# Kernel tuning notes

Measured on AMD Instinct MI355X. Metric: run time of the kernel, lower is better.

Reference implementation:

```python
import jax, jax.numpy as jnp
import numpy as np

N_NODES = 50000
N_EDGES = 800000
D = 128
N_GRAPHS = 64
N_CLASSES = 10


def setup_inputs() -> dict:
    key = jax.random.key(0)
    ks = jax.random.split(key, 10)
    x = jax.random.normal(ks[0], (N_NODES, D), dtype=jnp.float32)
    edge_index = jax.random.randint(ks[1], (2, N_EDGES), 0, N_NODES, dtype=jnp.int64)
    batch = jnp.sort(jax.random.randint(ks[2], (N_NODES,), 0, N_GRAPHS, dtype=jnp.int64))
    s = 1.0 / np.sqrt(D)
    W1a = jax.random.uniform(ks[3], (D, D), jnp.float32, -s, s)
    W1b = jax.random.uniform(ks[4], (D, D), jnp.float32, -s, s)
    W2a = jax.random.uniform(ks[5], (D, D), jnp.float32, -s, s)
    W2b = jax.random.uniform(ks[6], (D, D), jnp.float32, -s, s)
    Wfc = jax.random.uniform(ks[7], (D, N_CLASSES), jnp.float32, -s, s)
    return {
        "x": x, "edge_index": edge_index, "batch": batch,
        "W1a": W1a, "b1a": jnp.zeros((D,), jnp.float32),
        "W1b": W1b, "b1b": jnp.zeros((D,), jnp.float32),
        "W2a": W2a, "b2a": jnp.zeros((D,), jnp.float32),
        "W2b": W2b, "b2b": jnp.zeros((D,), jnp.float32),
        "Wfc": Wfc, "bfc": jnp.zeros((N_CLASSES,), jnp.float32),
    }


def _gin_conv(x, src, dst, Wa, ba, Wb, bb):
    # sum aggregation of neighbor messages x[src] into dst (eps = 0)
    agg = jax.ops.segment_sum(x[src], dst, num_segments=N_NODES)
    h = x + agg  # (1 + eps) * x + sum_{j->i} x_j
    h = jax.nn.relu(h @ Wa + ba)
    h = jax.nn.relu(h @ Wb + bb)
    return h


def reference(x, edge_index, batch, W1a, b1a, W1b, b1b, W2a, b2a, W2b, b2b, Wfc, bfc):
    src, dst = edge_index[0], edge_index[1]
    h = _gin_conv(x, src, dst, W1a, b1a, W1b, b1b)
    h = _gin_conv(h, src, dst, W2a, b2a, W2b, b2b)
    # global mean pool over graphs
    sums = jax.ops.segment_sum(h, batch, num_segments=N_GRAPHS)
    counts = jax.ops.segment_sum(jnp.ones((h.shape[0], 1), h.dtype), batch, num_segments=N_GRAPHS)
    pooled = sums / jnp.maximum(counts, 1.0)
    logits = pooled @ Wfc + bfc
    return jax.nn.sigmoid(logits)
```

## Files before the change

### kernel.cpp

```cpp
#include <hip/hip_runtime.h>

#define NN 50000
#define NE 800000
#define DF 128
#define NG 64
#define NC 10
#define NBK 98
#define PART_CHUNK 4096
#define PART_GRID 196
#define ACAP 12288
#define FINE_CAP 12288
#define RT 136
#define CAST_GRID 6250
#define PREP_GRID (CAST_GRID + 32)
#define POOL_GRID 391

typedef short bf16x8 __attribute__((ext_vector_type(8)));
typedef float f32x4  __attribute__((ext_vector_type(4)));

__device__ __forceinline__ void atomAddF(float* p, float v) {
  __hip_atomic_fetch_add(p, v, __ATOMIC_RELAXED, __HIP_MEMORY_SCOPE_AGENT);
}
__device__ __forceinline__ float b2f(unsigned short u) {
  union { unsigned int i; float f; } v; v.i = (unsigned int)u << 16; return v.f;
}
__device__ __forceinline__ unsigned int f2b(float f) {
  unsigned int i = __float_as_uint(f);
  return (i + 0x7fffu + ((i >> 16) & 1u)) >> 16;
}

__global__ __launch_bounds__(256) void k_prep_part(const float* __restrict__ x,
                                                   unsigned short* __restrict__ xb,
                                                   const float* __restrict__ W0,
                                                   const float* __restrict__ W1,
                                                   const float* __restrict__ W2,
                                                   const float* __restrict__ W3,
                                                   unsigned short* __restrict__ Wt,
                                                   const int* __restrict__ src,
                                                   const int* __restrict__ dst,
                                                   int* __restrict__ cnt_b,
                                                   unsigned int* __restrict__ arena)
{
  __shared__ unsigned int stage[PART_CHUNK];
  __shared__ int lhist[128], lcnt[128], lcur[128], gbase[128];
  const int tid = threadIdx.x;
  const int b   = blockIdx.x;

  if (b < CAST_GRID) {
    const int i = b * 256 + tid;
    const float4 v = reinterpret_cast<const float4*>(x)[i];
    uint2 o;
    o.x = f2b(v.x) | (f2b(v.y) << 16);
    o.y = f2b(v.z) | (f2b(v.w) << 16);
    reinterpret_cast<uint2*>(xb)[i] = o;
    return;
  }
  if (b < PREP_GRID) {
    const int o = (b - CAST_GRID) * 256 + tid;
    const int mat = o >> 11;
    const float* W = (mat == 0) ? W0 : (mat == 1) ? W1 : (mat == 2) ? W2 : W3;
    const int rem = o & 2047;
    const int kb = rem >> 7, n = rem & 127;
    unsigned int u[8];
#pragma unroll
    for (int j = 0; j < 8; ++j) u[j] = f2b(W[(size_t)(kb * 8 + j) * DF + n]);
    uint4 p;
    p.x = u[0] | (u[1] << 16);
    p.y = u[2] | (u[3] << 16);
    p.z = u[4] | (u[5] << 16);
    p.w = u[6] | (u[7] << 16);
    *reinterpret_cast<uint4*>(Wt + (size_t)mat * DF * DF + (size_t)rem * 8) = p;
    return;
  }

  const int vb = b - PREP_GRID;
  const int e0 = vb * PART_CHUNK;
  const int nE = min(PART_CHUNK, NE - e0);

  for (int i = tid; i < 128; i += 256) lhist[i] = 0;
  __syncthreads();
  unsigned int pk[16]; int bk[16];
#pragma unroll
  for (int i = 0; i < 16; ++i) {
    const int e = e0 + i * 256 + tid;
    if (e < NE) {
      const int d = dst[e], s = src[e];
      const int bb = d >> 9;
      bk[i] = bb;
      pk[i] = ((unsigned int)bb << 25) | ((unsigned int)(d & 511) << 16) | (unsigned int)s;
      atomicAdd(&lhist[bb], 1);
    } else bk[i] = -1;
  }
  __syncthreads();
  for (int i = tid; i < 128; i += 256) lcnt[i] = lhist[i];
  __syncthreads();
  for (int off = 1; off < 128; off <<= 1) {
    int v = 0;
    if (tid < 128 && tid >= off) v = lhist[tid - off];
    __syncthreads();
    if (tid < 128) lhist[tid] += v;
    __syncthreads();
  }
  if (tid < 128) lcur[tid] = lhist[tid] - lcnt[tid];
  __syncthreads();
#pragma unroll
  for (int i = 0; i < 16; ++i)
    if (bk[i] >= 0) {
      const int pos = atomicAdd(&lcur[bk[i]], 1);
      stage[pos] = pk[i];
    }
  __syncthreads();
  if (tid < NBK) {
    const int c = lcnt[tid];
    if (c > 0) gbase[tid] = atomicAdd(&cnt_b[tid], c);
  }
  __syncthreads();
  for (int idx = tid; idx < nE; idx += 256) {
    const unsigned int p = stage[idx];
    const int bb = (int)(p >> 25);
    const int loff = lhist[bb] - lcnt[bb];
    arena[(size_t)bb * ACAP + gbase[bb] + (idx - loff)] = p;
  }
}

__global__ __launch_bounds__(256) void k_fine(const unsigned int* __restrict__ arena,
                                              const int* __restrict__ cnt_b,
                                              int* __restrict__ rs,
                                              unsigned short* __restrict__ es)
{
  __shared__ unsigned short les[FINE_CAP];
  __shared__ int bins[4096];
  __shared__ int partials[256];
  __shared__ int basebuf[128];
  const int tid = threadIdx.x;
  const int b   = blockIdx.x;

  if (b == 0 && tid == 0) rs[NN] = NE;

  if (tid < 128) basebuf[tid] = (tid < NBK) ? cnt_b[tid] : 0;
  __syncthreads();
  for (int off = 1; off < 128; off <<= 1) {
    int u = 0;
    if (tid < 128 && tid >= off) u = basebuf[tid - off];
    __syncthreads();
    if (tid < 128) basebuf[tid] += u;
    __syncthreads();
  }
  const int wbase = (b == 0) ? 0 : basebuf[b - 1];
  const int cnt   = cnt_b[b];
  const int nbase = b << 9;
  const int nwin  = min(512, NN - nbase);
  const unsigned int* ap = arena + (size_t)b * ACAP;

  for (int i = tid; i < 4096; i += 256) bins[i] = 0;
  __syncthreads();
  for (int idx = tid; idx < cnt; idx += 256) {
    const unsigned int p = ap[idx];
    const int key = (int)(((p >> 16) & 511) << 3) | (int)((p & 0xffffu) >> 13);
    atomicAdd(&bins[key], 1);
  }
  __syncthreads();
  const int b16 = tid * 16;
  int sum = 0;
#pragma unroll
  for (int k = 0; k < 16; ++k) sum += bins[b16 + k];
  partials[tid] = sum;
  __syncthreads();
  for (int off = 1; off < 256; off <<= 1) {
    int u = (tid >= off) ? partials[tid - off] : 0;
    __syncthreads();
    partials[tid] += u;
    __syncthreads();
  }
  int run = partials[tid] - sum;
#pragma unroll
  for (int k = 0; k < 16; ++k) {
    const int v = bins[b16 + k];
    bins[b16 + k] = run;
    run += v;
  }
  __syncthreads();
  for (int i = tid; i < nwin; i += 256) rs[nbase + i] = wbase + bins[i << 3];
  __syncthreads();
  if (cnt <= FINE_CAP) {
    for (int idx = tid; idx < cnt; idx += 256) {
      const unsigned int p = ap[idx];
      const int key = (int)(((p >> 16) & 511) << 3) | (int)((p & 0xffffu) >> 13);
      const int pos = atomicAdd(&bins[key], 1);
      les[pos] = (unsigned short)(p & 0xffffu);
    }
    __syncthreads();
    for (int i = tid; i < cnt; i += 256) es[wbase + i] = les[i];
  } else {
    for (int idx = tid; idx < cnt; idx += 256) {
      const unsigned int p = ap[idx];
      const int key = (int)(((p >> 16) & 511) << 3) | (int)((p & 0xffffu) >> 13);
      const int pos = atomicAdd(&bins[key], 1);
      es[wbase + pos] = (unsigned short)(p & 0xffffu);
    }
  }
}

__global__ __launch_bounds__(256) void k_gather(const unsigned short* __restrict__ feat,
                                                unsigned short* __restrict__ outp,
                                                const int* __restrict__ rs,
                                                const unsigned short* __restrict__ es)
{
  const int wid  = (blockIdx.x * 256 + threadIdx.x) >> 6;
  const int lane = threadIdx.x & 63;
  if (wid >= NN) return;
  const int half = lane >> 5;
  const int l32  = lane & 31;
  const int off  = l32 * 4;
  const int beg = rs[wid];
  const int end = rs[wid + 1];

  float a0 = 0.f, a1 = 0.f, a2 = 0.f, a3 = 0.f;
  if (!half) {
    const uint2 u = *reinterpret_cast<const uint2*>(feat + (size_t)wid * DF + off);
    a0 = b2f(u.x & 0xffff); a1 = b2f(u.x >> 16);
    a2 = b2f(u.y & 0xffff); a3 = b2f(u.y >> 16);
  }

  int j = beg;
  for (; j + 7 < end; j += 8) {
    const int i0 = es[j + half];
    const int i1 = es[j + 2 + half];
    const int i2 = es[j + 4 + half];
    const int i3 = es[j + 6 + half];
    const uint2 u0 = *reinterpret_cast<const uint2*>(feat + (size_t)i0 * DF + off);
    const uint2 u1 = *reinterpret_cast<const uint2*>(feat + (size_t)i1 * DF + off);
    const uint2 u2 = *reinterpret_cast<const uint2*>(feat + (size_t)i2 * DF + off);
    const uint2 u3 = *reinterpret_cast<const uint2*>(feat + (size_t)i3 * DF + off);
    a0 += b2f(u0.x & 0xffff) + b2f(u1.x & 0xffff) + b2f(u2.x & 0xffff) + b2f(u3.x & 0xffff);
    a1 += b2f(u0.x >> 16)    + b2f(u1.x >> 16)    + b2f(u2.x >> 16)    + b2f(u3.x >> 16);
    a2 += b2f(u0.y & 0xffff) + b2f(u1.y & 0xffff) + b2f(u2.y & 0xffff) + b2f(u3.y & 0xffff);
    a3 += b2f(u0.y >> 16)    + b2f(u1.y >> 16)    + b2f(u2.y >> 16)    + b2f(u3.y >> 16);
  }
  for (; j + 1 < end; j += 2) {
    const int i = es[j + half];
    const uint2 u = *reinterpret_cast<const uint2*>(feat + (size_t)i * DF + off);
    a0 += b2f(u.x & 0xffff); a1 += b2f(u.x >> 16);
    a2 += b2f(u.y & 0xffff); a3 += b2f(u.y >> 16);
  }
  if (j < end && !half) {
    const int i = es[j];
    const uint2 u = *reinterpret_cast<const uint2*>(feat + (size_t)i * DF + off);
    a0 += b2f(u.x & 0xffff); a1 += b2f(u.x >> 16);
    a2 += b2f(u.y & 0xffff); a3 += b2f(u.y >> 16);
  }

  a0 += __shfl_xor(a0, 32);
  a1 += __shfl_xor(a1, 32);
  a2 += __shfl_xor(a2, 32);
  a3 += __shfl_xor(a3, 32);

  if (!half) {
    uint2 o;
    o.x = f2b(a0) | (f2b(a1) << 16);
    o.y = f2b(a2) | (f2b(a3) << 16);
    *reinterpret_cast<uint2*>(outp + (size_t)wid * DF + off) = o;
  }
}

__global__ __launch_bounds__(256, 4) void k_gemm2(const unsigned short* __restrict__ Ab,
                                                  const unsigned short* __restrict__ Wta,
                                                  const float* __restrict__ ba,
                                                  const unsigned short* __restrict__ Wtb,
                                                  const float* __restrict__ bb,
                                                  unsigned short* __restrict__ outb, int M)
{
  __shared__ unsigned short hL[4][16 * RT];
  const int tid  = threadIdx.x;
  const int lane = tid & 63;
  const int w    = tid >> 6;
  const int col  = lane & 15;
  const int kq   = lane >> 4;

  const int m   = blockIdx.x * 64 + w * 16 + col;
  const int mld = (m < M) ? m : (M - 1);

  bf16x8 bc[4];
#pragma unroll
  for (int s = 0; s < 4; ++s)
    bc[s] = *reinterpret_cast<const bf16x8*>(Ab + (size_t)mld * DF + s * 32 + kq * 8);

  f32x4 acc[8];
#pragma unroll
  for (int nf = 0; nf < 8; ++nf) acc[nf] = (f32x4){0.f, 0.f, 0.f, 0.f};
#pragma unroll
  for (int s = 0; s < 4; ++s) {
#pragma unroll
    for (int nf = 0; nf < 8; ++nf) {
      const bf16x8 wa = *reinterpret_cast<const bf16x8*>(
          Wta + ((size_t)(s * 4 + kq) * 128 + nf * 16 + col) * 8);
      acc[nf] = __builtin_amdgcn_mfma_f32_16x16x32_bf16(wa, bc[s], acc[nf], 0, 0, 0);
    }
  }

  unsigned short* hw = &hL[w][0];
#pragma unroll
  for (int nf = 0; nf < 8; ++nf) {
    const float4 bva = *reinterpret_cast<const float4*>(ba + nf * 16 + kq * 4);
    uint2 pk;
    pk.x = f2b(fmaxf(acc[nf][0] + bva.x, 0.f)) | (f2b(fmaxf(acc[nf][1] + bva.y, 0.f)) << 16);
    pk.y = f2b(fmaxf(acc[nf][2] + bva.z, 0.f)) | (f2b(fmaxf(acc[nf][3] + bva.w, 0.f)) << 16);
    *reinterpret_cast<uint2*>(&hw[col * RT + nf * 16 + kq * 4]) = pk;
  }

  f32x4 acc2[8];
#pragma unroll
  for (int nf = 0; nf < 8; ++nf) acc2[nf] = (f32x4){0.f, 0.f, 0.f, 0.f};
#pragma unroll
  for (int s = 0; s < 4; ++s) {
    const bf16x8 hb = *reinterpret_cast<const bf16x8*>(&hw[col * RT + s * 32 + kq * 8]);
#pragma unroll
    for (int nf = 0; nf < 8; ++nf) {
      const bf16x8 wb = *reinterpret_cast<const bf16x8*>(
          Wtb + ((size_t)(s * 4 + kq) * 128 + nf * 16 + col) * 8);
      acc2[nf] = __builtin_amdgcn_mfma_f32_16x16x32_bf16(wb, hb, acc2[nf], 0, 0, 0);
    }
  }
  if (m < M) {
#pragma unroll
    for (int nf = 0; nf < 8; ++nf) {
      const float4 bvb = *reinterpret_cast<const float4*>(bb + nf * 16 + kq * 4);
      ushort4 p;
      p.x = (unsigned short)f2b(fmaxf(acc2[nf][0] + bvb.x, 0.f));
      p.y = (unsigned short)f2b(fmaxf(acc2[nf][1] + bvb.y, 0.f));
      p.z = (unsigned short)f2b(fmaxf(acc2[nf][2] + bvb.z, 0.f));
      p.w = (unsigned short)f2b(fmaxf(acc2[nf][3] + bvb.w, 0.f));
      *reinterpret_cast<ushort4*>(outb + (size_t)m * DF + nf * 16 + kq * 4) = p;
    }
  }
}

__global__ __launch_bounds__(256) void k_pool(const unsigned short* __restrict__ h,
                                              const int* __restrict__ batch,
                                              float* __restrict__ sums,
                                              int* __restrict__ cnts)
{
  const int wv   = (blockIdx.x * 256 + threadIdx.x) >> 6;
  const int lane = threadIdx.x & 63;
  const int n0 = wv * 32;
  if (n0 >= NN) return;
  const int n1 = min(n0 + 32, NN);
  const int off = lane * 2;

  const int gfirst = batch[n0];
  const int glast  = batch[n1 - 1];
  float ax = 0.f, ay = 0.f;

  if (gfirst == glast) {
#pragma unroll 4
    for (int i = n0; i < n1; ++i) {
      const unsigned int u = *reinterpret_cast<const unsigned int*>(h + (size_t)i * DF + off);
      ax += b2f(u & 0xffff); ay += b2f(u >> 16);
    }
    atomAddF(&sums[gfirst * DF + off],     ax);
    atomAddF(&sums[gfirst * DF + off + 1], ay);
    if (lane == 0) atomicAdd(&cnts[gfirst], n1 - n0);
  } else {
    int g = gfirst, cnt = 0;
    for (int i = n0; i < n1; ++i) {
      const int gi = batch[i];
      if (gi != g) {
        atomAddF(&sums[g * DF + off],     ax);
        atomAddF(&sums[g * DF + off + 1], ay);
        if (lane == 0) atomicAdd(&cnts[g], cnt);
        ax = 0.f; ay = 0.f; cnt = 0; g = gi;
      }
      const unsigned int u = *reinterpret_cast<const unsigned int*>(h + (size_t)i * DF + off);
      ax += b2f(u & 0xffff); ay += b2f(u >> 16);
      ++cnt;
    }
    atomAddF(&sums[g * DF + off],     ax);
    atomAddF(&sums[g * DF + off + 1], ay);
    if (lane == 0) atomicAdd(&cnts[g], cnt);
  }
}

__global__ __launch_bounds__(256) void k_head(const float* __restrict__ sums,
                                              const int* __restrict__ cnts,
                                              const float* __restrict__ Wfc,
                                              const float* __restrict__ bfc,
                                              float* __restrict__ out)
{
  const int o = blockIdx.x * 256 + threadIdx.x;
  if (o >= NG * NC) return;
  const int g = o / NC, c = o % NC;
  const float inv = 1.f / fmaxf((float)cnts[g], 1.f);
  float z = bfc[c];
#pragma unroll 8
  for (int k = 0; k < DF; ++k)
    z = fmaf(sums[g * DF + k] * inv, Wfc[k * NC + c], z);
  out[o] = 1.f / (1.f + expf(-z));
}

extern "C" void kernel_launch(void* const* d_in, const int* in_sizes, int n_in,
                              void* d_out, int out_size, void* d_ws, size_t ws_size,
                              hipStream_t stream)
{
  const float* x   = (const float*)d_in[0];
  const int*   ei  = (const int*)d_in[1];
  const int* batch = (const int*)d_in[2];
  const float* W1a = (const float*)d_in[3];
  const float* b1a = (const float*)d_in[4];
  const float* W1b = (const float*)d_in[5];
  const float* b1b = (const float*)d_in[6];
  const float* W2a = (const float*)d_in[7];
  const float* b2a = (const float*)d_in[8];
  const float* W2b = (const float*)d_in[9];
  const float* b2b = (const float*)d_in[10];
  const float* Wfc = (const float*)d_in[11];
  const float* bfc = (const float*)d_in[12];
  float* out = (float*)d_out;

  const int* src = ei;
  const int* dst = ei + NE;

  unsigned short* xb = (unsigned short*)d_ws;
  unsigned short* A  = xb + (size_t)NN * DF;
  unsigned short* H  = A + (size_t)NN * DF;
  unsigned short* Wt = H + (size_t)NN * DF;
  float* sums  = (float*)(Wt + (size_t)4 * DF * DF);
  int*   cnts  = (int*)(sums + NG * DF);
  int*   cnt_b = cnts + 64;
  int*   rs    = cnt_b + 128;
  unsigned short* es = (unsigned short*)(rs + (NN + 4));
  unsigned int* arena = (unsigned int*)(es + NE);

  unsigned short* Wt1a = Wt;
  unsigned short* Wt1b = Wt + DF * DF;
  unsigned short* Wt2a = Wt + 2 * DF * DF;
  unsigned short* Wt2b = Wt + 3 * DF * DF;

  const int gemm_grid   = (NN + 63) / 64;
  const int gather_grid = (NN * 64 + 255) / 256;

  hipMemsetAsync(sums, 0, (size_t)(NG * DF + 64 + 128) * sizeof(float), stream);
  k_prep_part<<<PREP_GRID + PART_GRID, 256, 0, stream>>>(
      x, xb, W1a, W1b, W2a, W2b, Wt, src, dst, cnt_b, arena);
  k_fine<<<NBK, 256, 0, stream>>>(arena, cnt_b, rs, es);

  k_gather<<<gather_grid, 256, 0, stream>>>(xb, A, rs, es);
  k_gemm2<<<gemm_grid, 256, 0, stream>>>(A, Wt1a, b1a, Wt1b, b1b, A, NN);

  k_gather<<<gather_grid, 256, 0, stream>>>(A, H, rs, es);
  k_gemm2<<<gemm_grid, 256, 0, stream>>>(H, Wt2a, b2a, Wt2b, b2b, H, NN);

  k_pool<<<POOL_GRID, 256, 0, stream>>>(H, batch, sums, cnts);
  k_head<<<(NG * NC + 255) / 256, 256, 0, stream>>>(sums, cnts, Wfc, bfc, out);
}
```

Baseline: 183.0 us.

## Fuse neighbor gather into MLP GEMM kernel via shared-memory staging

Merges the gather/aggregation kernel and the two-layer MLP GEMM kernel into one conv kernel per layer. Each wave aggregates 16 nodes serially into LDS and then runs the MFMA GEMMs straight from LDS. This removes the round trip of the aggregated features through global memory and one launch per layer. In exchange each wave walks its 16 nodes one after another, so there are 4x fewer waves in flight for the latency-bound gather, which may hurt memory-level parallelism. For nodes past NN, LDS rows are left unwritten but their outputs are never stored.

After: 205.8 us. 12.4% more time.

```diff
diff --git a/kernel.cpp b/kernel.cpp
--- a/kernel.cpp
+++ b/kernel.cpp
@@ -201,74 +201,14 @@
   }
 }
 
-__global__ __launch_bounds__(256) void k_gather(const unsigned short* __restrict__ feat,
-                                                unsigned short* __restrict__ outp,
-                                                const int* __restrict__ rs,
-                                                const unsigned short* __restrict__ es)
-{
-  const int wid  = (blockIdx.x * 256 + threadIdx.x) >> 6;
-  const int lane = threadIdx.x & 63;
-  if (wid >= NN) return;
-  const int half = lane >> 5;
-  const int l32  = lane & 31;
-  const int off  = l32 * 4;
-  const int beg = rs[wid];
-  const int end = rs[wid + 1];
-
-  float a0 = 0.f, a1 = 0.f, a2 = 0.f, a3 = 0.f;
-  if (!half) {
-    const uint2 u = *reinterpret_cast<const uint2*>(feat + (size_t)wid * DF + off);
-    a0 = b2f(u.x & 0xffff); a1 = b2f(u.x >> 16);
-    a2 = b2f(u.y & 0xffff); a3 = b2f(u.y >> 16);
-  }
-
-  int j = beg;
-  for (; j + 7 < end; j += 8) {
-    const int i0 = es[j + half];
-    const int i1 = es[j + 2 + half];
-    const int i2 = es[j + 4 + half];
-    const int i3 = es[j + 6 + half];
-    const uint2 u0 = *reinterpret_cast<const uint2*>(feat + (size_t)i0 * DF + off);
-    const uint2 u1 = *reinterpret_cast<const uint2*>(feat + (size_t)i1 * DF + off);
-    const uint2 u2 = *reinterpret_cast<const uint2*>(feat + (size_t)i2 * DF + off);
-    const uint2 u3 = *reinterpret_cast<const uint2*>(feat + (size_t)i3 * DF + off);
-    a0 += b2f(u0.x & 0xffff) + b2f(u1.x & 0xffff) + b2f(u2.x & 0xffff) + b2f(u3.x & 0xffff);
-    a1 += b2f(u0.x >> 16)    + b2f(u1.x >> 16)    + b2f(u2.x >> 16)    + b2f(u3.x >> 16);
-    a2 += b2f(u0.y & 0xffff) + b2f(u1.y & 0xffff) + b2f(u2.y & 0xffff) + b2f(u3.y & 0xffff);
-    a3 += b2f(u0.y >> 16)    + b2f(u1.y >> 16)    + b2f(u2.y >> 16)    + b2f(u3.y >> 16);
-  }
-  for (; j + 1 < end; j += 2) {
-    const int i = es[j + half];
-    const uint2 u = *reinterpret_cast<const uint2*>(feat + (size_t)i * DF + off);
-    a0 += b2f(u.x & 0xffff); a1 += b2f(u.x >> 16);
-    a2 += b2f(u.y & 0xffff); a3 += b2f(u.y >> 16);
-  }
-  if (j < end && !half) {
-    const int i = es[j];
-    const uint2 u = *reinterpret_cast<const uint2*>(feat + (size_t)i * DF + off);
-    a0 += b2f(u.x & 0xffff); a1 += b2f(u.x >> 16);
-    a2 += b2f(u.y & 0xffff); a3 += b2f(u.y >> 16);
-  }
-
-  a0 += __shfl_xor(a0, 32);
-  a1 += __shfl_xor(a1, 32);
-  a2 += __shfl_xor(a2, 32);
-  a3 += __shfl_xor(a3, 32);
-
-  if (!half) {
-    uint2 o;
-    o.x = f2b(a0) | (f2b(a1) << 16);
-    o.y = f2b(a2) | (f2b(a3) << 16);
-    *reinterpret_cast<uint2*>(outp + (size_t)wid * DF + off) = o;
-  }
-}
-
-__global__ __launch_bounds__(256, 4) void k_gemm2(const unsigned short* __restrict__ Ab,
-                                                  const unsigned short* __restrict__ Wta,
-                                                  const float* __restrict__ ba,
-                                                  const unsigned short* __restrict__ Wtb,
-                                                  const float* __restrict__ bb,
-                                                  unsigned short* __restrict__ outb, int M)
+__global__ __launch_bounds__(256, 4) void k_conv(const unsigned short* __restrict__ feat,
+                                                 const int* __restrict__ rs,
+                                                 const unsigned short* __restrict__ es,
+                                                 const unsigned short* __restrict__ Wta,
+                                                 const float* __restrict__ ba,
+                                                 const unsigned short* __restrict__ Wtb,
+                                                 const float* __restrict__ bb,
+                                                 unsigned short* __restrict__ outb)
 {
   __shared__ unsigned short hL[4][16 * RT];
   const int tid  = threadIdx.x;
@@ -276,14 +216,68 @@
   const int w    = tid >> 6;
   const int col  = lane & 15;
   const int kq   = lane >> 4;
-
-  const int m   = blockIdx.x * 64 + w * 16 + col;
-  const int mld = (m < M) ? m : (M - 1);
+  const int half = lane >> 5;
+  const int l32  = lane & 31;
+  const int offg = l32 * 4;
+
+  unsigned short* hw = &hL[w][0];
+  const int base = blockIdx.x * 64 + w * 16;
+
+  for (int r = 0; r < 16; ++r) {
+    const int node = base + r;
+    if (node >= NN) break;
+    const int beg = rs[node];
+    const int end = rs[node + 1];
+
+    float a0 = 0.f, a1 = 0.f, a2 = 0.f, a3 = 0.f;
+    if (!half) {
+      const uint2 u = *reinterpret_cast<const uint2*>(feat + (size_t)node * DF + offg);
+      a0 = b2f(u.x & 0xffff); a1 = b2f(u.x >> 16);
+      a2 = b2f(u.y & 0xffff); a3 = b2f(u.y >> 16);
+    }
+    int j = beg;
+    for (; j + 7 < end; j += 8) {
+      const int i0 = es[j + half];
+      const int i1 = es[j + 2 + half];
+      const int i2 = es[j + 4 + half];
+      const int i3 = es[j + 6 + half];
+      const uint2 u0 = *reinterpret_cast<const uint2*>(feat + (size_t)i0 * DF + offg);
+      const uint2 u1 = *reinterpret_cast<const uint2*>(feat + (size_t)i1 * DF + offg);
+      const uint2 u2 = *reinterpret_cast<const uint2*>(feat + (size_t)i2 * DF + offg);
+      const uint2 u3 = *reinterpret_cast<const uint2*>(feat + (size_t)i3 * DF + offg);
+      a0 += b2f(u0.x & 0xffff) + b2f(u1.x & 0xffff) + b2f(u2.x & 0xffff) + b2f(u3.x & 0xffff);
+      a1 += b2f(u0.x >> 16)    + b2f(u1.x >> 16)    + b2f(u2.x >> 16)    + b2f(u3.x >> 16);
+      a2 += b2f(u0.y & 0xffff) + b2f(u1.y & 0xffff) + b2f(u2.y & 0xffff) + b2f(u3.y & 0xffff);
+      a3 += b2f(u0.y >> 16)    + b2f(u1.y >> 16)    + b2f(u2.y >> 16)    + b2f(u3.y >> 16);
+    }
+    for (; j + 1 < end; j += 2) {
+      const int i = es[j + half];
+      const uint2 u = *reinterpret_cast<const uint2*>(feat + (size_t)i * DF + offg);
+      a0 += b2f(u.x & 0xffff); a1 += b2f(u.x >> 16);
+      a2 += b2f(u.y & 0xffff); a3 += b2f(u.y >> 16);
+    }
+    if (j < end && !half) {
+      const int i = es[j];
+      const uint2 u = *reinterpret_cast<const uint2*>(feat + (size_t)i * DF + offg);
+      a0 += b2f(u.x & 0xffff); a1 += b2f(u.x >> 16);
+      a2 += b2f(u.y & 0xffff); a3 += b2f(u.y >> 16);
+    }
+    a0 += __shfl_xor(a0, 32);
+    a1 += __shfl_xor(a1, 32);
+    a2 += __shfl_xor(a2, 32);
+    a3 += __shfl_xor(a3, 32);
+    if (!half) {
+      uint2 o;
+      o.x = f2b(a0) | (f2b(a1) << 16);
+      o.y = f2b(a2) | (f2b(a3) << 16);
+      *reinterpret_cast<uint2*>(&hw[r * RT + offg]) = o;
+    }
+  }
 
   bf16x8 bc[4];
 #pragma unroll
   for (int s = 0; s < 4; ++s)
-    bc[s] = *reinterpret_cast<const bf16x8*>(Ab + (size_t)mld * DF + s * 32 + kq * 8);
+    bc[s] = *reinterpret_cast<const bf16x8*>(&hw[col * RT + s * 32 + kq * 8]);
 
   f32x4 acc[8];
 #pragma unroll
@@ -298,7 +292,6 @@
     }
   }
 
-  unsigned short* hw = &hL[w][0];
 #pragma unroll
   for (int nf = 0; nf < 8; ++nf) {
     const float4 bva = *reinterpret_cast<const float4*>(ba + nf * 16 + kq * 4);
@@ -321,7 +314,8 @@
       acc2[nf] = __builtin_amdgcn_mfma_f32_16x16x32_bf16(wb, hb, acc2[nf], 0, 0, 0);
     }
   }
-  if (m < M) {
+  const int m = base + col;
+  if (m < NN) {
 #pragma unroll
     for (int nf = 0; nf < 8; ++nf) {
       const float4 bvb = *reinterpret_cast<const float4*>(bb + nf * 16 + kq * 4);
@@ -435,19 +429,16 @@
   unsigned short* Wt2a = Wt + 2 * DF * DF;
   unsigned short* Wt2b = Wt + 3 * DF * DF;
 
-  const int gemm_grid   = (NN + 63) / 64;
-  const int gather_grid = (NN * 64 + 255) / 256;
+  const int conv_grid = (NN + 63) / 64;
 
   hipMemsetAsync(sums, 0, (size_t)(NG * DF + 64 + 128) * sizeof(float), stream);
   k_prep_part<<<PREP_GRID + PART_GRID, 256, 0, stream>>>(
       x, xb, W1a, W1b, W2a, W2b, Wt, src, dst, cnt_b, arena);
   k_fine<<<NBK, 256, 0, stream>>>(arena, cnt_b, rs, es);
 
-  k_gather<<<gather_grid, 256, 0, stream>>>(xb, A, rs, es);
-  k_gemm2<<<gemm_grid, 256, 0, stream>>>(A, Wt1a, b1a, Wt1b, b1b, A, NN);
-
-  k_gather<<<gather_grid, 256, 0, stream>>>(A, H, rs, es);
-  k_gemm2<<<gemm_grid, 256, 0, stream>>>(H, Wt2a, b2a, Wt2b, b2b, H, NN);
+  k_conv<<<conv_grid, 256, 0, stream>>>(xb, rs, es, Wt1a, b1a, Wt1b, b1b, A);
+
+  k_conv<<<conv_grid, 256, 0, stream>>>(A, rs, es, Wt2a, b2a, Wt2b, b2b, H);
 
   k_pool<<<POOL_GRID, 256, 0, stream>>>(H, batch, sums, cnts);
   k_head<<<(NG * NC + 255) / 256, 256, 0, stream>>>(sums, cnts, Wfc, bfc, out);
```
